# Kernel tuning notes

Hardware: AMD Instinct MI355X
Metric: run time of the kernel (lower is better)

The kernel has to match this reference:

```python
import jax, jax.numpy as jnp
import numpy as np

B, T, H, L = 64, 1024, 256, 1


def setup_inputs() -> dict:
    key = jax.random.key(0)
    ks = jax.random.split(key, 20)
    s = 1.0 / np.sqrt(H)

    def u(k, shape):
        return jax.random.uniform(k, shape, jnp.float32, -s, s)

    return {
        "inputs": jax.random.normal(ks[0], (B, T, H), jnp.float32),
        "hidden_states": jax.random.normal(ks[1], (L, B, H), jnp.float32),
        # Attn params: W is Linear(2H -> H), V is Linear(H -> H)
        "W_w": u(ks[2], (H, 2 * H)), "W_b": u(ks[3], (H,)),
        "V_w": u(ks[4], (H, H)), "V_b": u(ks[5], (H,)),
        # GRU params (input_size == hidden_size)
        "w_ir": u(ks[6], (H, H)), "w_iz": u(ks[7], (H, H)), "w_in": u(ks[8], (H, H)),
        "b_ir": u(ks[9], (H,)), "b_iz": u(ks[10], (H,)), "b_in": u(ks[11], (H,)),
        "w_hr": u(ks[12], (H, H)), "w_hz": u(ks[13], (H, H)), "w_hn": u(ks[14], (H, H)),
        "b_hr": u(ks[15], (H,)), "b_hz": u(ks[16], (H,)), "b_hn": u(ks[17], (H,)),
    }


def reference(inputs, hidden_states, W_w, W_b, V_w, V_b,
              w_ir, w_iz, w_in, b_ir, b_iz, b_in,
              w_hr, w_hz, w_hn, b_hr, b_hz, b_hn):
    h = inputs.shape[-1]
    # ---- Attn: score_t = sum_l V(tanh(W([h_l ; x_t]))) ----
    # Split W over the concat: first H cols act on hidden, last H on input.
    W_hid, W_inp = W_w[:, :h], W_w[:, h:]
    hp = jnp.einsum('lbh,kh->lbk', hidden_states, W_hid)      # (L,B,H)
    xp = jnp.einsum('bth,kh->tbk', inputs, W_inp)             # (T,B,H)
    z = jnp.tanh(hp[:, None] + xp[None] + W_b)                # (L,T,B,H)
    scores = jnp.einsum('ltbh,kh->tbk', z, V_w) + inputs.shape[0] * 0.0  # (T,B,H) pre-bias
    scores = scores + V_b * hidden_states.shape[0]            # V bias summed over L layers
    scores = jnp.swapaxes(scores, 0, 1)                       # (B,T,H)
    sm = jax.nn.softmax(scores, axis=1)                       # softmax over seq dim
    ctx = scores * sm                                         # (B,T,H) attention-weighted features
    x_attn = sm.sum(axis=2)                                   # (B,T)

    # ---- GRU over ctx (faithful: outputs[0]=h0, recurrence starts at t=1) ----
    h0 = hidden_states[0]                                     # (B,H)
    xr = jnp.einsum('bth,kh->tbk', ctx, w_ir) + b_ir          # (T,B,H)
    xz = jnp.einsum('bth,kh->tbk', ctx, w_iz) + b_iz
    xn = jnp.einsum('bth,kh->tbk', ctx, w_in) + b_in

    def step(h_prev, xs):
        xr_t, xz_t, xn_t = xs
        r = jax.nn.sigmoid(xr_t + h_prev @ w_hr.T + b_hr)
        n = jnp.tanh(xn_t + r * (h_prev @ w_hn.T + b_hn))
        zt = jax.nn.sigmoid(xz_t + h_prev @ w_hz.T + b_hz)
        h_new = (1.0 - zt) * n + zt * h_prev
        return h_new, h_new

    h_last, hs = jax.lax.scan(step, h0, (xr[1:], xz[1:], xn[1:]))
    outs = jnp.concatenate([h0[None], hs], axis=0)            # (T,B,H)
    outputs = jnp.swapaxes(outs, 0, 1)                        # (B,T,H)
    return outputs, h_last[None], x_attn
```

## Files before the change

### kernel.cpp

```cpp
#include <hip/hip_runtime.h>

#define DEVI __device__ __forceinline__

typedef float  f32x4  __attribute__((ext_vector_type(4)));
typedef __bf16 bf16x8 __attribute__((ext_vector_type(8)));
typedef unsigned short u16x8 __attribute__((ext_vector_type(8)));

DEVI unsigned short f2bf(float f) {
    unsigned u = __builtin_bit_cast(unsigned, f);
    unsigned r = (u + 0x7fffu + ((u >> 16) & 1u)) >> 16;
    return (unsigned short)r;
}
DEVI float bf2f(unsigned short s) {
    return __builtin_bit_cast(float, (unsigned)s << 16);
}
DEVI u16x8 pack8(float4 a, float4 b) {
    u16x8 p;
    p[0] = f2bf(a.x); p[1] = f2bf(a.y); p[2] = f2bf(a.z); p[3] = f2bf(a.w);
    p[4] = f2bf(b.x); p[5] = f2bf(b.y); p[6] = f2bf(b.z); p[7] = f2bf(b.w);
    return p;
}
DEVI f32x4 mfma16(u16x8 a, u16x8 b, f32x4 c) {
    return __builtin_amdgcn_mfma_f32_16x16x32_bf16(
        __builtin_bit_cast(bf16x8, a), __builtin_bit_cast(bf16x8, b), c, 0, 0, 0);
}
DEVI float sigm(float x)   { return 1.f / (1.f + __expf(-x)); }
DEVI float tanh_f(float x) { return 1.f - 2.f / (1.f + __expf(2.f * x)); }

#define Hh 256
#define Bb 64
#define Tt 1024
#define MROWS (Bb * Tt)

__global__ __launch_bounds__(256) void hp_kernel(const float* __restrict__ hid,
                                                 const float* __restrict__ Ww,
                                                 float* __restrict__ hp) {
    int b = blockIdx.x, k = threadIdx.x;
    __shared__ __align__(16) float hs[Hh];
    hs[k] = hid[b * Hh + k];
    __syncthreads();
    const float4* w4 = (const float4*)(Ww + (size_t)k * 512);
    const float4* h4 = (const float4*)hs;
    float acc = 0.f;
#pragma unroll 8
    for (int i = 0; i < 64; i++) {
        float4 a = w4[i], x = h4[i];
        acc += a.x * x.x + a.y * x.y + a.z * x.z + a.w * x.w;
    }
    hp[b * Hh + k] = acc;
}

__global__ __launch_bounds__(256) void bias_prep(const float* __restrict__ b_ir,
                                                 const float* __restrict__ b_hr,
                                                 const float* __restrict__ b_iz,
                                                 const float* __restrict__ b_hz,
                                                 float* __restrict__ cb) {
    int k = threadIdx.x;
    cb[k] = b_ir[k] + b_hr[k];
    cb[256 + k] = b_iz[k] + b_hz[k];
}

template <int EPI, bool ABF16>
__global__ __launch_bounds__(512) void gemm_k(
    const void* __restrict__ Aab,
    const float* __restrict__ W0, const float* __restrict__ W1, const float* __restrict__ W2,
    int wstride, int wcoloff,
    const float* __restrict__ bv0, const float* __restrict__ bv1, const float* __restrict__ bv2,
    const float* __restrict__ hp, const float* __restrict__ Wb,
    void* __restrict__ outv) {
    __shared__ __align__(16) unsigned short As[128 * 256];
    __shared__ __align__(16) unsigned short Bs[64 * 256];

    int tid = threadIdx.x;
    int bx = blockIdx.x, by = blockIdx.y;
    int mat = (EPI == 2) ? (by >> 2) : 0;
    int cb  = (EPI == 2) ? (by & 3) : by;
    int rowBase = bx * 128, colBase = cb * 64;
    const float* W  = (mat == 0) ? W0 : ((mat == 1) ? W1 : W2);
    const float* bv = (mat == 0) ? bv0 : ((mat == 1) ? bv1 : bv2);

    if (ABF16) {
        const unsigned short* A = (const unsigned short*)Aab;
#pragma unroll
        for (int i = 0; i < 8; i++) {
            int idx = i * 512 + tid, r = idx >> 5, g = idx & 31, gs = g ^ (r & 7);
            *(uint4*)&As[r * 256 + gs * 8] =
                *(const uint4*)(A + (((size_t)(rowBase + r)) << 8) + g * 8);
        }
    } else {
        const float* A = (const float*)Aab;
#pragma unroll
        for (int i = 0; i < 8; i++) {
            int idx = i * 512 + tid, r = idx >> 5, g = idx & 31, gs = g ^ (r & 7);
            const float* s = A + (((size_t)(rowBase + r)) << 8) + g * 8;
            float4 f0 = *(const float4*)s, f1 = *(const float4*)(s + 4);
            *(u16x8*)&As[r * 256 + gs * 8] = pack8(f0, f1);
        }
    }
#pragma unroll
    for (int i = 0; i < 4; i++) {
        int idx = i * 512 + tid, r = idx >> 5, g = idx & 31, gs = g ^ (r & 7);
        const float* s = W + (size_t)(colBase + r) * wstride + wcoloff + g * 8;
        float4 f0 = *(const float4*)s, f1 = *(const float4*)(s + 4);
        *(u16x8*)&Bs[r * 256 + gs * 8] = pack8(f0, f1);
    }
    __syncthreads();

    int wid = tid >> 6, lane = tid & 63, l15 = lane & 15, grp = lane >> 4;
    int wr = (wid >> 1) * 32, wc = (wid & 1) * 32;
    f32x4 acc[2][2] = {};
#pragma unroll
    for (int kc = 0; kc < 8; kc++) {
        u16x8 a[2], bb[2];
#pragma unroll
        for (int rt = 0; rt < 2; rt++) {
            int r = wr + rt * 16 + l15;
            int gs = (kc * 4 + grp) ^ (r & 7);
            a[rt] = *(const u16x8*)&As[r * 256 + gs * 8];
        }
#pragma unroll
        for (int ct = 0; ct < 2; ct++) {
            int r = wc + ct * 16 + l15;
            int gs = (kc * 4 + grp) ^ (r & 7);
            bb[ct] = *(const u16x8*)&Bs[r * 256 + gs * 8];
        }
#pragma unroll
        for (int rt = 0; rt < 2; rt++)
#pragma unroll
            for (int ct = 0; ct < 2; ct++)
                acc[rt][ct] = mfma16(a[rt], bb[ct], acc[rt][ct]);
    }
#pragma unroll
    for (int rt = 0; rt < 2; rt++)
#pragma unroll
        for (int ct = 0; ct < 2; ct++)
#pragma unroll
            for (int i = 0; i < 4; i++) {
                int rl = wr + rt * 16 + grp * 4 + i;
                int cl = wc + ct * 16 + l15;
                size_t r = (size_t)rowBase + rl;
                int c = colBase + cl;
                float v = acc[rt][ct][i];
                if (EPI == 0) {
                    v = tanh_f(v + hp[(r >> 10) * 256 + c] + Wb[c]);
                    ((unsigned short*)outv)[r * 256 + c] = f2bf(v);
                } else if (EPI == 1) {
                    ((float*)outv)[r * 256 + c] = v + bv[c];
                } else {
                    size_t t = r & 1023, b = r >> 10;
                    ((unsigned short*)outv)[(size_t)mat * 16777216 + (t * 64 + b) * 256 + c] =
                        f2bf(v + bv[c]);
                }
            }
}

__global__ __launch_bounds__(256) void softmax_pass1(const float* __restrict__ scores,
                                                     float* __restrict__ partMS) {
    int b = blockIdx.x, tc = blockIdx.y, k = threadIdx.x;
    const float* p = scores + ((size_t)b * Tt + tc * 128) * Hh + k;
    float m = -1e30f, S = 0.f;
    for (int i = 0; i < 128; i++) {
        float s = p[(size_t)i * Hh];
        float mn = fmaxf(m, s);
        S = S * __expf(m - mn) + __expf(s - mn);
        m = mn;
    }
    int idx = (b * 8 + tc) * Hh + k;
    partMS[idx * 2] = m;
    partMS[idx * 2 + 1] = S;
}

__global__ __launch_bounds__(256) void softmax_pass2(const float* __restrict__ scores,
                                                     const float* __restrict__ partMS,
                                                     unsigned short* __restrict__ ctx,
                                                     float* __restrict__ x_attn) {
    int b = blockIdx.x, tc = blockIdx.y;
    int tid = threadIdx.x, w = tid >> 6, lane = tid & 63;
    float mj[4], Sj[4];
#pragma unroll
    for (int j = 0; j < 4; j++) {
        int k = lane + j * 64;
        float m = -1e30f;
#pragma unroll
        for (int c = 0; c < 8; c++)
            m = fmaxf(m, partMS[((b * 8 + c) * Hh + k) * 2]);
        float S = 0.f;
#pragma unroll
        for (int c = 0; c < 8; c++) {
            int idx = (b * 8 + c) * Hh + k;
            S += partMS[idx * 2 + 1] * __expf(partMS[idx * 2] - m);
        }
        mj[j] = m;
        Sj[j] = 1.f / S;
    }
    for (int i = 0; i < 32; i++) {
        int t = tc * 128 + w * 32 + i;
        const float* sp = scores + ((size_t)b * Tt + t) * Hh;
        unsigned short* cp = ctx + ((size_t)b * Tt + t) * Hh;
        float accsm = 0.f;
#pragma unroll
        for (int j = 0; j < 4; j++) {
            int k = lane + j * 64;
            float s = sp[k];
            float sm = __expf(s - mj[j]) * Sj[j];
            accsm += sm;
            cp[k] = f2bf(s * sm);
        }
#pragma unroll
        for (int o = 32; o >= 1; o >>= 1) accsm += __shfl_xor(accsm, o, 64);
        if (lane == 0) x_attn[b * Tt + t] = accsm;
    }
}

__global__ __attribute__((amdgpu_flat_work_group_size(512, 512),
                          amdgpu_waves_per_eu(2, 2)))
void scan_gru(
    const unsigned short* __restrict__ xg,
    const float* __restrict__ whr, const float* __restrict__ whz, const float* __restrict__ whn,
    const float* __restrict__ bhn,
    const float* __restrict__ hidden,
    float* __restrict__ outputs, float* __restrict__ hlast) {
    __shared__ __align__(16) unsigned short wn_lds[65536];
    __shared__ __align__(16) unsigned short hb[2][Hh];
    int b = blockIdx.x;
    int tid = threadIdx.x, w = tid >> 6, lane = tid & 63;
    int grp = lane >> 4;

    for (int it = 0; it < 16; ++it) {
        int q = it * 512 + tid;
        int frag = q >> 6, lslot = q & 63;
        int col = ((frag >> 3) << 4) | (lslot & 15);
        int koff = (frag & 7) * 32 + (lslot >> 4) * 8;
        const float* s = whn + (size_t)col * Hh + koff;
        *(u16x8*)&wn_lds[frag * 512 + lslot * 8] = pack8(*(const float4*)s, *(const float4*)(s + 4));
    }

    u16x8 wfr[2][8], wfz[2][8];
#pragma unroll
    for (int ct = 0; ct < 2; ct++) {
        int col = w * 32 + ct * 16 + (lane & 15);
#pragma unroll
        for (int kc = 0; kc < 8; kc++) {
            const float* s1 = whr + (size_t)col * Hh + kc * 32 + grp * 8;
            wfr[ct][kc] = pack8(*(const float4*)s1, *(const float4*)(s1 + 4));
            const float* s2 = whz + (size_t)col * Hh + kc * 32 + grp * 8;
            wfz[ct][kc] = pack8(*(const float4*)s2, *(const float4*)(s2 + 4));
        }
    }
    asm volatile("" : "+a"(wfr[0][0]), "+a"(wfr[0][1]), "+a"(wfr[0][2]), "+a"(wfr[0][3]),
                      "+a"(wfr[0][4]), "+a"(wfr[0][5]), "+a"(wfr[0][6]), "+a"(wfr[0][7]));
    asm volatile("" : "+a"(wfr[1][0]), "+a"(wfr[1][1]), "+a"(wfr[1][2]), "+a"(wfr[1][3]),
                      "+a"(wfr[1][4]), "+a"(wfr[1][5]), "+a"(wfr[1][6]), "+a"(wfr[1][7]));
    asm volatile("" : "+a"(wfz[0][0]), "+a"(wfz[0][1]), "+a"(wfz[0][2]), "+a"(wfz[0][3]),
                      "+a"(wfz[0][4]), "+a"(wfz[0][5]), "+a"(wfz[0][6]), "+a"(wfz[0][7]));
    asm volatile("" : "+a"(wfz[1][0]), "+a"(wfz[1][1]), "+a"(wfz[1][2]), "+a"(wfz[1][3]),
                      "+a"(wfz[1][4]), "+a"(wfz[1][5]), "+a"(wfz[1][6]), "+a"(wfz[1][7]));

    int mycol = w * 32 + (lane & 31);
    int wnb = (w * 16) * 512 + lane * 8;
    float bhnS = 0.f, hpS = 0.f;
    if (lane < 32) {
        bhnS = bhn[mycol];
        hpS = hidden[b * Hh + mycol];
        hb[0][mycol] = f2bf(hpS);
        outputs[((size_t)b * Tt) * Hh + mycol] = hpS;
    }
    const unsigned short* xr = xg;
    const unsigned short* xz = xg + 16777216;
    const unsigned short* xn = xg + 33554432;
    unsigned short pxr = 0, pxz = 0, pxn = 0;
    if (lane < 32) {
        size_t off = ((size_t)64 + b) * Hh + mycol;
        pxr = xr[off]; pxz = xz[off]; pxn = xn[off];
    }
    __syncthreads();

    int p = 0;
    for (int t = 1; t < Tt; t++) {
        unsigned short cxr = pxr, cxz = pxz, cxn = pxn;
        int tnext = (t + 1 < Tt) ? t + 1 : t;
        if (lane < 32) {
            size_t off = ((size_t)tnext * 64 + b) * Hh + mycol;
            pxr = xr[off]; pxz = xz[off]; pxn = xn[off];
        }
        f32x4 ar0 = {0.f, 0.f, 0.f, 0.f}, ar1 = {0.f, 0.f, 0.f, 0.f};
        f32x4 az0 = {0.f, 0.f, 0.f, 0.f}, az1 = {0.f, 0.f, 0.f, 0.f};
        f32x4 an0 = {0.f, 0.f, 0.f, 0.f}, an1 = {0.f, 0.f, 0.f, 0.f};
#pragma unroll
        for (int kc = 0; kc < 8; kc++) {
            u16x8 af = *(const u16x8*)&hb[p][kc * 32 + grp * 8];
            ar0 = mfma16(af, wfr[0][kc], ar0);
            ar1 = mfma16(af, wfr[1][kc], ar1);
            az0 = mfma16(af, wfz[0][kc], az0);
            az1 = mfma16(af, wfz[1][kc], az1);
            u16x8 wn0 = *(const u16x8*)&wn_lds[wnb + kc * 512];
            u16x8 wn1 = *(const u16x8*)&wn_lds[wnb + 8 * 512 + kc * 512];
            an0 = mfma16(af, wn0, an0);
            an1 = mfma16(af, wn1, an1);
        }
        float vr = __shfl(ar1[0], lane & 15);
        float vz = __shfl(az1[0], lane & 15);
        float vn = __shfl(an1[0], lane & 15);
        float gr = (lane < 16) ? ar0[0] : vr;
        float gz = (lane < 16) ? az0[0] : vz;
        float gn = (lane < 16) ? an0[0] : vn;
        if (lane < 32) {
            float r0 = sigm(bf2f(cxr) + gr);
            float z0 = sigm(bf2f(cxz) + gz);
            float n0 = tanh_f(bf2f(cxn) + r0 * (gn + bhnS));
            float hn = (1.f - z0) * n0 + z0 * hpS;
            hb[p ^ 1][mycol] = f2bf(hn);
            outputs[((size_t)b * Tt + t) * Hh + mycol] = hn;
            hpS = hn;
        }
        p ^= 1;
        asm volatile("s_waitcnt lgkmcnt(0)" ::: "memory");
        __builtin_amdgcn_s_barrier();
        asm volatile("" ::: "memory");
    }
    if (lane < 32) {
        hlast[b * Hh + mycol] = hpS;
    }
}

extern "C" void kernel_launch(void* const* d_in, const int* in_sizes, int n_in,
                              void* d_out, int out_size, void* d_ws, size_t ws_size,
                              hipStream_t stream) {
    const float* inputs = (const float*)d_in[0];
    const float* hidden = (const float*)d_in[1];
    const float* W_w  = (const float*)d_in[2];
    const float* W_b  = (const float*)d_in[3];
    const float* V_w  = (const float*)d_in[4];
    const float* V_b  = (const float*)d_in[5];
    const float* w_ir = (const float*)d_in[6];
    const float* w_iz = (const float*)d_in[7];
    const float* w_in = (const float*)d_in[8];
    const float* b_ir = (const float*)d_in[9];
    const float* b_iz = (const float*)d_in[10];
    const float* b_in = (const float*)d_in[11];
    const float* w_hr = (const float*)d_in[12];
    const float* w_hz = (const float*)d_in[13];
    const float* w_hn = (const float*)d_in[14];
    const float* b_hr = (const float*)d_in[15];
    const float* b_hz = (const float*)d_in[16];
    const float* b_hn = (const float*)d_in[17];

    float* hp = (float*)d_ws;
    float* partMS = hp + 65536;
    float* cbias = partMS + 262144;
    unsigned short* zbuf = (unsigned short*)(cbias + 512);
    unsigned short* ctx = zbuf;
    unsigned short* xgb = zbuf + 16777216;

    float* scores  = (float*)d_out;
    float* outputs = (float*)d_out;
    float* hlast   = outputs + 16777216;
    float* x_attn  = hlast + 16384;

    hp_kernel<<<64, 256, 0, stream>>>(hidden, W_w, hp);
    bias_prep<<<1, 256, 0, stream>>>(b_ir, b_hr, b_iz, b_hz, cbias);

    gemm_k<0, false><<<dim3(512, 4), 512, 0, stream>>>(
        inputs, W_w, nullptr, nullptr, 512, 256,
        nullptr, nullptr, nullptr, hp, W_b, zbuf);

    gemm_k<1, true><<<dim3(512, 4), 512, 0, stream>>>(
        zbuf, V_w, nullptr, nullptr, 256, 0,
        V_b, nullptr, nullptr, nullptr, nullptr, scores);

    softmax_pass1<<<dim3(64, 8), 256, 0, stream>>>(scores, partMS);
    softmax_pass2<<<dim3(64, 8), 256, 0, stream>>>(scores, partMS, ctx, x_attn);

    gemm_k<2, true><<<dim3(512, 12), 512, 0, stream>>>(
        ctx, w_ir, w_iz, w_in, 256, 0,
        cbias, cbias + 256, b_in, nullptr, nullptr, xgb);

    scan_gru<<<64, 512, 0, stream>>>(
        xgb, w_hr, w_hz, w_hn, b_hn, hidden, outputs, hlast);
}
```

Before: 1.477 ms.

## Fuse softmax partial max/sum into score GEMM epilogue and keep gate layout batch-major

```diff
diff --git a/kernel.cpp b/kernel.cpp
--- a/kernel.cpp
+++ b/kernel.cpp
@@ -67,9 +67,11 @@
     int wstride, int wcoloff,
     const float* __restrict__ bv0, const float* __restrict__ bv1, const float* __restrict__ bv2,
     const float* __restrict__ hp, const float* __restrict__ Wb,
+    float* __restrict__ pms,
     void* __restrict__ outv) {
     __shared__ __align__(16) unsigned short As[128 * 256];
     __shared__ __align__(16) unsigned short Bs[64 * 256];
+    __shared__ float sredm[8][2][16], sredS[8][2][16];
 
     int tid = threadIdx.x;
     int bx = blockIdx.x, by = blockIdx.y;
@@ -130,6 +132,7 @@
             for (int ct = 0; ct < 2; ct++)
                 acc[rt][ct] = mfma16(a[rt], bb[ct], acc[rt][ct]);
     }
+    float vv[2][2][4];
 #pragma unroll
     for (int rt = 0; rt < 2; rt++)
 #pragma unroll
@@ -145,29 +148,59 @@
                     v = tanh_f(v + hp[(r >> 10) * 256 + c] + Wb[c]);
                     ((unsigned short*)outv)[r * 256 + c] = f2bf(v);
                 } else if (EPI == 1) {
-                    ((float*)outv)[r * 256 + c] = v + bv[c];
+                    float sc = v + bv[c];
+                    vv[rt][ct][i] = sc;
+                    ((float*)outv)[r * 256 + c] = sc;
                 } else {
-                    size_t t = r & 1023, b = r >> 10;
-                    ((unsigned short*)outv)[(size_t)mat * 16777216 + (t * 64 + b) * 256 + c] =
+                    ((unsigned short*)outv)[(size_t)mat * 16777216 + r * 256 + c] =
                         f2bf(v + bv[c]);
                 }
             }
-}
-
-__global__ __launch_bounds__(256) void softmax_pass1(const float* __restrict__ scores,
-                                                     float* __restrict__ partMS) {
-    int b = blockIdx.x, tc = blockIdx.y, k = threadIdx.x;
-    const float* p = scores + ((size_t)b * Tt + tc * 128) * Hh + k;
-    float m = -1e30f, S = 0.f;
-    for (int i = 0; i < 128; i++) {
-        float s = p[(size_t)i * Hh];
-        float mn = fmaxf(m, s);
-        S = S * __expf(m - mn) + __expf(s - mn);
-        m = mn;
-    }
-    int idx = (b * 8 + tc) * Hh + k;
-    partMS[idx * 2] = m;
-    partMS[idx * 2 + 1] = S;
+    if constexpr (EPI == 1) {
+        int b_ = rowBase >> 10, tc_ = (rowBase >> 7) & 7;
+#pragma unroll
+        for (int ct = 0; ct < 2; ct++) {
+            float m = vv[0][ct][0];
+#pragma unroll
+            for (int rt = 0; rt < 2; rt++)
+#pragma unroll
+                for (int i = 0; i < 4; i++) m = fmaxf(m, vv[rt][ct][i]);
+            float S = 0.f;
+#pragma unroll
+            for (int rt = 0; rt < 2; rt++)
+#pragma unroll
+                for (int i = 0; i < 4; i++) S += __expf(vv[rt][ct][i] - m);
+#pragma unroll
+            for (int o = 16; o <= 32; o <<= 1) {
+                float om = __shfl_xor(m, o, 64);
+                float oS = __shfl_xor(S, o, 64);
+                float nm = fmaxf(m, om);
+                S = S * __expf(m - nm) + oS * __expf(om - nm);
+                m = nm;
+            }
+            if (grp == 0) {
+                sredm[wid][ct][l15] = m;
+                sredS[wid][ct][l15] = S;
+            }
+        }
+        __syncthreads();
+        if (tid < 64) {
+            int cl = tid;
+            int wcol = cl >> 5, ct = (cl >> 4) & 1, k15 = cl & 15;
+            float m = -1e30f, S = 0.f;
+#pragma unroll
+            for (int rg = 0; rg < 4; rg++) {
+                float om = sredm[rg * 2 + wcol][ct][k15];
+                float oS = sredS[rg * 2 + wcol][ct][k15];
+                float nm = fmaxf(m, om);
+                S = S * __expf(m - nm) + oS * __expf(om - nm);
+                m = nm;
+            }
+            int idx = (b_ * 8 + tc_) * Hh + colBase + cl;
+            pms[idx * 2] = m;
+            pms[idx * 2 + 1] = S;
+        }
+    }
 }
 
 __global__ __launch_bounds__(256) void softmax_pass2(const float* __restrict__ scores,
@@ -270,7 +303,7 @@
     const unsigned short* xn = xg + 33554432;
     unsigned short pxr = 0, pxz = 0, pxn = 0;
     if (lane < 32) {
-        size_t off = ((size_t)64 + b) * Hh + mycol;
+        size_t off = ((size_t)b * Tt + 1) * Hh + mycol;
         pxr = xr[off]; pxz = xz[off]; pxn = xn[off];
     }
     __syncthreads();
@@ -280,7 +313,7 @@
         unsigned short cxr = pxr, cxz = pxz, cxn = pxn;
         int tnext = (t + 1 < Tt) ? t + 1 : t;
         if (lane < 32) {
-            size_t off = ((size_t)tnext * 64 + b) * Hh + mycol;
+            size_t off = ((size_t)b * Tt + tnext) * Hh + mycol;
             pxr = xr[off]; pxz = xz[off]; pxn = xn[off];
         }
         f32x4 ar0 = {0.f, 0.f, 0.f, 0.f}, ar1 = {0.f, 0.f, 0.f, 0.f};
@@ -362,18 +395,17 @@
 
     gemm_k<0, false><<<dim3(512, 4), 512, 0, stream>>>(
         inputs, W_w, nullptr, nullptr, 512, 256,
-        nullptr, nullptr, nullptr, hp, W_b, zbuf);
+        nullptr, nullptr, nullptr, hp, W_b, nullptr, zbuf);
 
     gemm_k<1, true><<<dim3(512, 4), 512, 0, stream>>>(
         zbuf, V_w, nullptr, nullptr, 256, 0,
-        V_b, nullptr, nullptr, nullptr, nullptr, scores);
-
-    softmax_pass1<<<dim3(64, 8), 256, 0, stream>>>(scores, partMS);
+        V_b, nullptr, nullptr, nullptr, nullptr, partMS, scores);
+
     softmax_pass2<<<dim3(64, 8), 256, 0, stream>>>(scores, partMS, ctx, x_attn);
 
     gemm_k<2, true><<<dim3(512, 12), 512, 0, stream>>>(
         ctx, w_ir, w_iz, w_in, 256, 0,
-        cbias, cbias + 256, b_in, nullptr, nullptr, xgb);
+        cbias, cbias + 256, b_in, nullptr, nullptr, nullptr, xgb);
 
     scan_gru<<<64, 512, 0, stream>>>(
         xgb, w_hr, w_hz, w_hn, b_hn, hidden, outputs, hlast);
```

Result: no change. 1.454 ms (-1.5%).
